# Kernel tuning notes

Measured on AMD Instinct MI355X. Metric: run time of the kernel, lower is better.

## Reference

```python
import jax, jax.numpy as jnp
import numpy as np

K = 3
TOPK = 32
TELEPORT = 0.1
LN_EPS = 1e-5


def _block(x, ln_g, ln_b, w1, b1, w2, b2, log_tau, gate):
    residual = x
    # pre: LayerNorm -> Linear -> GELU (exact erf, torch default)
    mu = jnp.mean(x, axis=-1, keepdims=True)
    var = jnp.mean(jnp.square(x - mu), axis=-1, keepdims=True)
    h = (x - mu) * jax.lax.rsqrt(var + LN_EPS) * ln_g + ln_b
    h = jax.nn.gelu(h @ w1 + b1, approximate=False)  # [B, N, H]

    # dynamic cosine adjacency with top-k sparsification
    tau = jnp.maximum(jnp.exp(log_tau), 1e-3)
    xn = h / jnp.maximum(jnp.linalg.norm(h, axis=-1, keepdims=True), 1e-12)
    A = jnp.maximum(jnp.einsum('bnf,bmf->bnm', xn, xn), 0.0)  # [B, N, N]
    B, N, _ = A.shape
    vals, idx = jax.lax.top_k(A, TOPK)  # idx: [B, N, TOPK]
    bi = jnp.arange(B)[:, None, None]
    ni = jnp.arange(N)[None, :, None]
    mask = jnp.zeros(A.shape, dtype=bool).at[bi, ni, idx].set(True)
    I = jnp.eye(N, dtype=A.dtype)
    A = jnp.where(mask, A, 0.0) + I
    A = A / tau

    # teleport + symmetric degree normalization
    A = (1.0 - TELEPORT) * A + TELEPORT * I
    deg = jnp.maximum(A.sum(-1), 1e-6)  # [B, N]
    dm12 = deg ** -0.5
    Ahat = dm12[:, :, None] * A * dm12[:, None, :]

    # Chebyshev propagation
    T0 = h
    outs = [T0]
    if K > 1:
        T1 = jnp.einsum('bnm,bmf->bnf', Ahat, T0)
        outs.append(T1)
    for _ in range(2, K):
        outs.append(2.0 * jnp.einsum('bnm,bmf->bnf', Ahat, outs[-1]) - outs[-2])
    hcat = jnp.concatenate(outs, axis=-1)  # [B, N, H*K]
    y = hcat @ w2 + b2
    return residual + jnp.tanh(gate) * y


def setup_inputs() -> dict:
    key = jax.random.key(0)
    k0, k1, k2 = jax.random.split(key, 3)
    Bsz, N, D, H, O = 4, 4096, 128, 128, 128
    x = jax.random.normal(k0, (Bsz, N, D), dtype=jnp.float32)
    ln_g = jnp.ones((D,), jnp.float32)
    ln_b = jnp.zeros((D,), jnp.float32)
    w1 = jax.random.normal(k1, (D, H), jnp.float32) / np.float32(np.sqrt(D))
    b1 = jnp.zeros((H,), jnp.float32)
    w2 = jax.random.normal(k2, (H * K, O), jnp.float32) / np.float32(np.sqrt(H * K))
    b2 = jnp.zeros((O,), jnp.float32)
    log_tau = jnp.asarray(np.log(0.5), jnp.float32)
    gate = jnp.asarray(0.2, jnp.float32)
    return {"x": x, "ln_g": ln_g, "ln_b": ln_b, "w1": w1, "b1": b1,
            "w2": w2, "b2": b2, "log_tau": log_tau, "gate": gate}


def reference(x, ln_g, ln_b, w1, b1, w2, b2, log_tau, gate):
    return _block(x, ln_g, ln_b, w1, b1, w2, b2, log_tau, gate)
```

## Files before the change

kernel.cpp:

```cpp
#include <hip/hip_runtime.h>
#include <hip/hip_bf16.h>
#include <stdint.h>

#define NB 4
#define NN 4096

using f16x8 = __attribute__((ext_vector_type(8))) _Float16;
using f32x4 = __attribute__((ext_vector_type(4))) float;

__device__ __forceinline__ float wave_sum(float v) {
  #pragma unroll
  for (int o = 32; o > 0; o >>= 1) v += __shfl_xor(v, o, 64);
  return v;
}
__device__ __forceinline__ float h2f_bits(unsigned hb) {
  unsigned short us = (unsigned short)hb;
  _Float16 hf;
  __builtin_memcpy(&hf, &us, 2);
  return (float)hf;
}
__device__ __forceinline__ unsigned short f2h_bits(float f) {
  _Float16 hf = (_Float16)f;
  unsigned short us;
  __builtin_memcpy(&us, &hf, 2);
  return us;
}
__device__ __forceinline__ unsigned pack2h(float lo, float hi) {
  return ((unsigned)f2h_bits(hi) << 16) | (unsigned)f2h_bits(lo);
}

#define INS16(c) do { unsigned t_;                      \
  t_ = max(l0, c);  c = min(l0, c);  l0 = t_;           \
  t_ = max(l1, c);  c = min(l1, c);  l1 = t_;           \
  t_ = max(l2, c);  c = min(l2, c);  l2 = t_;           \
  t_ = max(l3, c);  c = min(l3, c);  l3 = t_;           \
  t_ = max(l4, c);  c = min(l4, c);  l4 = t_;           \
  t_ = max(l5, c);  c = min(l5, c);  l5 = t_;           \
  t_ = max(l6, c);  c = min(l6, c);  l6 = t_;           \
  t_ = max(l7, c);  c = min(l7, c);  l7 = t_;           \
  t_ = max(l8, c);  c = min(l8, c);  l8 = t_;           \
  t_ = max(l9, c);  c = min(l9, c);  l9 = t_;           \
  t_ = max(l10, c); c = min(l10, c); l10 = t_;          \
  t_ = max(l11, c); c = min(l11, c); l11 = t_;          \
  t_ = max(l12, c); c = min(l12, c); l12 = t_;          \
  t_ = max(l13, c); c = min(l13, c); l13 = t_;          \
  t_ = max(l14, c); c = min(l14, c); l14 = t_;          \
  l15 = max(l15, c);                                    \
} while (0)

#define SHIFT_L() do { l0=l1; l1=l2; l2=l3; l3=l4; l4=l5; l5=l6; l6=l7; l7=l8; \
  l8=l9; l9=l10; l10=l11; l11=l12; l12=l13; l13=l14; l14=l15; l15=0; } while (0)
#define SHIFT_P() do { p0=p1; p1=p2; p2=p3; p3=p4; p4=p5; p5=p6; p6=p7; p7=p8; \
  p8=p9; p9=p10; p10=p11; p11=p12; p12=p13; p13=p14; p14=p15; p15=0; } while (0)

__global__ __launch_bounds__(128) void k_prepw(
    const float* __restrict__ w1, const float* __restrict__ w2,
    _Float16* __restrict__ w1t16, _Float16* __restrict__ w2t16) {
  int n = blockIdx.x;
  int t = threadIdx.x;
  __shared__ _Float16 v16[128];
  __shared__ float v[384];
  v16[t] = (_Float16)w1[(size_t)t * 128 + n];
  #pragma unroll
  for (int i = 0; i < 3; ++i) v[i * 128 + t] = w2[(size_t)(i * 128 + t) * 128 + n];
  __syncthreads();
  if (t < 16) {
    union { _Float16 hh[8]; uint4 u; } pk;
    #pragma unroll
    for (int j = 0; j < 8; ++j) pk.hh[j] = v16[t * 8 + j];
    *(uint4*)(w1t16 + (size_t)n * 128 + (size_t)(t ^ (n & 7)) * 8) = pk.u;
  }
  if (t < 48) {
    int kc = t >> 4, cl = t & 15;
    union { _Float16 hh[8]; uint4 u; } pk;
    #pragma unroll
    for (int e = 0; e < 8; ++e) pk.hh[e] = (_Float16)v[t * 8 + e];
    *(uint4*)(w2t16 + (size_t)n * 384 + kc * 128 + (size_t)(cl ^ (n & 7)) * 8) = pk.u;
  }
}

__global__ __launch_bounds__(256) void k0_ln(
    const float* __restrict__ x, const float* __restrict__ ln_g,
    const float* __restrict__ ln_b, _Float16* __restrict__ ln16) {
  int lane = threadIdx.x & 63;
  int row = blockIdx.x * 4 + (threadIdx.x >> 6);
  float2 xv = ((const float2*)x)[(size_t)row * 64 + lane];
  float2 gv = ((const float2*)ln_g)[lane];
  float2 bv = ((const float2*)ln_b)[lane];
  float mu = wave_sum(xv.x + xv.y) * (1.0f / 128.0f);
  float dx = xv.x - mu, dy = xv.y - mu;
  float var = wave_sum(dx * dx + dy * dy) * (1.0f / 128.0f);
  float ri = 1.0f / sqrtf(var + 1e-5f);
  float h0 = dx * ri * gv.x + bv.x;
  float h1 = dy * ri * gv.y + bv.y;
  int c = lane >> 2;
  int addr = row * 128 + ((c ^ (row & 7)) << 3) + (lane & 3) * 2;
  *(unsigned*)(ln16 + addr) = pack2h(h0, h1);
}

__global__ __launch_bounds__(256) void k1_mfma(
    const _Float16* __restrict__ ln16, const _Float16* __restrict__ w1t16,
    const float* __restrict__ b1, _Float16* __restrict__ h16,
    _Float16* __restrict__ hn16) {
  __shared__ _Float16 As[64 * 128];
  __shared__ _Float16 Bs[128 * 128];
  int tid = threadIdx.x;
  int lane = tid & 63;
  int wv = tid >> 6;
  int rbase = blockIdx.x * 64;
  #pragma unroll
  for (int i = 0; i < 4; ++i) {
    int idx = tid + 256 * i;
    __builtin_amdgcn_global_load_lds(
        (const __attribute__((address_space(1))) void*)(ln16 + (size_t)rbase * 128 + (size_t)idx * 8),
        (__attribute__((address_space(3))) void*)(As + (size_t)idx * 8), 16, 0, 0);
  }
  #pragma unroll
  for (int i = 0; i < 8; ++i) {
    int idx = tid + 256 * i;
    __builtin_amdgcn_global_load_lds(
        (const __attribute__((address_space(1))) void*)(w1t16 + (size_t)idx * 8),
        (__attribute__((address_space(3))) void*)(Bs + (size_t)idx * 8), 16, 0, 0);
  }
  asm volatile("s_waitcnt vmcnt(0)" ::: "memory");
  __syncthreads();

  int rl = lane & 15, kg = lane >> 4;
  f32x4 acc[8];
  #pragma unroll
  for (int j = 0; j < 8; ++j) acc[j] = (f32x4){0.f, 0.f, 0.f, 0.f};
  #pragma unroll
  for (int kk = 0; kk < 4; ++kk) {
    int cL = kk * 4 + kg;
    int r = wv * 16 + rl;
    f16x8 a = *(const f16x8*)(As + r * 128 + (cL ^ (r & 7)) * 8);
    #pragma unroll
    for (int j = 0; j < 8; ++j) {
      int n = j * 16 + rl;
      f16x8 bf = *(const f16x8*)(Bs + n * 128 + (cL ^ (n & 7)) * 8);
      acc[j] = __builtin_amdgcn_mfma_f32_16x16x32_f16(a, bf, acc[j], 0, 0, 0);
    }
  }
  float ssq[4] = {0.f, 0.f, 0.f, 0.f};
  #pragma unroll
  for (int j = 0; j < 8; ++j) {
    float bv = b1[j * 16 + rl];
    #pragma unroll
    for (int rg = 0; rg < 4; ++rg) {
      float z = acc[j][rg] + bv;
      float g = 0.5f * z * (1.0f + erff(z * 0.70710678118654752440f));
      acc[j][rg] = g;
      ssq[rg] += g * g;
    }
  }
  #pragma unroll
  for (int o = 1; o < 16; o <<= 1)
    #pragma unroll
    for (int rg = 0; rg < 4; ++rg) ssq[rg] += __shfl_xor(ssq[rg], o, 64);
  float rinv[4];
  #pragma unroll
  for (int rg = 0; rg < 4; ++rg) rinv[rg] = 1.0f / fmaxf(sqrtf(ssq[rg]), 1e-12f);

  #pragma unroll
  for (int j = 0; j < 8; ++j) {
    #pragma unroll
    for (int rg = 0; rg < 4; ++rg) {
      float g = acc[j][rg];
      float gp = __shfl_xor(g, 1, 64);
      if ((rl & 1) == 0) {
        int row = rbase + wv * 16 + kg * 4 + rg;
        int col = j * 16 + rl;
        int c = col >> 3;
        int ad = row * 128 + (((c ^ (row & 7))) << 3) + (col & 7);
        *(unsigned*)(h16 + ad) = pack2h(g, gp);
        *(unsigned*)(hn16 + ad) = pack2h(g * rinv[rg], gp * rinv[rg]);
      }
    }
  }
}

__global__ __launch_bounds__(512, 1) void k_scores_topk(
    const _Float16* __restrict__ hn16, int* __restrict__ nidx,
    float* __restrict__ nval, float* __restrict__ dm12,
    const float* __restrict__ p_log_tau) {
  __shared__ _Float16 Qs[64 * 128];
  __shared__ _Float16 Cs[2][2][64 * 128];
  __shared__ unsigned stk[16 * 512];
  int tid = threadIdx.x;
  int lane = tid & 63;
  int wv = tid >> 6;
  int g = wv >> 2;
  int wq = wv & 3;
  int rl = lane & 15, kg = lane >> 4;
  int t = tid & 255;
  int blk = blockIdx.x;
  int b = blk >> 6;
  int qbase = (blk & 63) * 64;
  const _Float16* hb = hn16 + (size_t)b * NN * 128;

  #pragma unroll
  for (int i = 0; i < 2; ++i) {
    int idx = tid + 512 * i;
    __builtin_amdgcn_global_load_lds(
        (const __attribute__((address_space(1))) void*)(hb + (size_t)qbase * 128 + (size_t)idx * 8),
        (__attribute__((address_space(3))) void*)(Qs + (size_t)idx * 8), 16, 0, 0);
  }
  const _Float16* cw = hb + (size_t)(g * 2048) * 128;
  #pragma unroll
  for (int i = 0; i < 4; ++i) {
    int idx = t + 256 * i;
    __builtin_amdgcn_global_load_lds(
        (const __attribute__((address_space(1))) void*)(cw + (size_t)idx * 8),
        (__attribute__((address_space(3))) void*)(&Cs[g][0][0] + (size_t)idx * 8), 16, 0, 0);
  }
  asm volatile("s_waitcnt vmcnt(0)" ::: "memory");
  __syncthreads();

  int qrow = wq * 16 + rl;
  f16x8 bq[4];
  #pragma unroll
  for (int kk = 0; kk < 4; ++kk)
    bq[kk] = *(const f16x8*)(Qs + qrow * 128 + ((kk * 4 + kg) ^ (qrow & 7)) * 8);

  unsigned l0 = 0, l1 = 0, l2 = 0, l3 = 0, l4 = 0, l5 = 0, l6 = 0, l7 = 0,
           l8 = 0, l9 = 0, l10 = 0, l11 = 0, l12 = 0, l13 = 0, l14 = 0, l15 = 0;
  unsigned gate = 0;

  for (int cb = 0; cb < 32; ++cb) {
    int cur = cb & 1;
    if (cb < 31) {
      const _Float16* csrc = cw + (size_t)(cb + 1) * 64 * 128;
      #pragma unroll
      for (int i = 0; i < 4; ++i) {
        int idx = t + 256 * i;
        __builtin_amdgcn_global_load_lds(
            (const __attribute__((address_space(1))) void*)(csrc + (size_t)idx * 8),
            (__attribute__((address_space(3))) void*)(&Cs[g][cur ^ 1][0] + (size_t)idx * 8), 16, 0, 0);
      }
    }
    f32x4 acc[4];
    #pragma unroll
    for (int j = 0; j < 4; ++j) acc[j] = (f32x4){0.f, 0.f, 0.f, 0.f};
    #pragma unroll
    for (int kk = 0; kk < 4; ++kk) {
      #pragma unroll
      for (int j = 0; j < 4; ++j) {
        int mrow = j * 16 + rl;
        f16x8 a = *(const f16x8*)(&Cs[g][cur][0] + mrow * 128 + ((kk * 4 + kg) ^ (rl & 7)) * 8);
        acc[j] = __builtin_amdgcn_mfma_f32_16x16x32_f16(a, bq[kk], acc[j], 0, 0, 0);
      }
    }
    int cnt = 0;
    int kb = 4095 - (g * 2048 + cb * 64 + kg * 4);
    #pragma unroll
    for (int j = 0; j < 4; ++j) {
      #pragma unroll
      for (int rg = 0; rg < 4; ++rg) {
        float v = fmaxf(acc[j][rg], 0.0f);
        unsigned key = ((unsigned)f2h_bits(v) << 16) | (unsigned)(kb - j * 16 - rg);
        if (key > gate) {
          stk[cnt * 512 + tid] = key;
          ++cnt;
        }
      }
    }
    int wm = cnt;
    #pragma unroll
    for (int o = 1; o < 64; o <<= 1) {
      int w = __shfl_xor(wm, o, 64);
      wm = max(wm, w);
    }
    if (wm > 0) {
      unsigned nxt = stk[tid];
      for (int i = 0; i < wm; ++i) {
        unsigned c = (i < cnt) ? nxt : 0u;
        nxt = stk[(unsigned)min(i + 1, 15) * 512 + tid];
        INS16(c);
      }
      unsigned m7 = min(l7, (unsigned)__shfl_xor((int)l7, 16, 64));
      m7 = min(m7, (unsigned)__shfl_xor((int)m7, 32, 64));
      gate = max(l15, m7);
    }
    asm volatile("s_waitcnt vmcnt(0)" ::: "memory");
    __syncthreads();
  }

  if (g == 1) {
    unsigned* dst = stk + (((wq * 16 + rl) * 4 + kg) * 16);
    *(uint4*)(dst + 0)  = (uint4){l0, l1, l2, l3};
    *(uint4*)(dst + 4)  = (uint4){l4, l5, l6, l7};
    *(uint4*)(dst + 8)  = (uint4){l8, l9, l10, l11};
    *(uint4*)(dst + 12) = (uint4){l12, l13, l14, l15};
  }
  __syncthreads();
  if (g == 0) {
    const unsigned* src = stk + (((wq * 16 + rl) * 4 + kg) * 16);
    uint4 pa = *(const uint4*)(src + 0);
    uint4 pb = *(const uint4*)(src + 4);
    uint4 pc = *(const uint4*)(src + 8);
    uint4 pd = *(const uint4*)(src + 12);
    unsigned p0 = pa.x, p1 = pa.y, p2 = pa.z, p3 = pa.w;
    unsigned p4 = pb.x, p5 = pb.y, p6 = pb.z, p7 = pb.w;
    unsigned p8 = pc.x, p9 = pc.y, p10 = pc.z, p11 = pc.w;
    unsigned p12 = pd.x, p13 = pd.y, p14 = pd.z, p15 = pd.w;

    unsigned sv[8];
    float sum = 0.0f;
    #pragma unroll
    for (int e = 0; e < 32; ++e) {
      unsigned v = max(l0, p0);
      v = max(v, (unsigned)__shfl_xor((int)v, 16, 64));
      v = max(v, (unsigned)__shfl_xor((int)v, 32, 64));
      if (l0 == v) { SHIFT_L(); }
      else if (p0 == v) { SHIFT_P(); }
      sum += h2f_bits(v >> 16);
      if (kg == (e & 3)) sv[e >> 2] = v;
    }
    int grow = b * NN + qbase + qrow;
    #pragma unroll
    for (int s = 0; s < 8; ++s) {
      unsigned v = sv[s];
      nidx[(size_t)grow * 32 + s * 4 + kg] = 4095 - (int)(v & 0xFFFu);
      nval[(size_t)grow * 32 + s * 4 + kg] = h2f_bits(v >> 16);
    }
    if (kg == 0) {
      float tau = fmaxf(expf(p_log_tau[0]), 1e-3f);
      float deg = fmaxf(0.9f * ((sum + 1.0f) / tau) + 0.1f, 1e-6f);
      dm12[grow] = 1.0f / sqrtf(deg);
    }
  }
}

__global__ __launch_bounds__(128) void k_cheb1(
    const _Float16* __restrict__ h16, const int* __restrict__ nidx,
    const float* __restrict__ nval, const float* __restrict__ dm12,
    const float* __restrict__ p_log_tau, _Float16* __restrict__ T116) {
  int row = blockIdx.x;
  int b = row >> 12;
  int tid = threadIdx.x;
  __shared__ float cj[32];
  __shared__ int mj[32];
  __shared__ float cdsh;
  float tau = fmaxf(expf(p_log_tau[0]), 1e-3f);
  float scale = 0.9f / tau;
  float dn = dm12[row];
  if (tid < 32) {
    int m = nidx[(size_t)row * 32 + tid];
    cj[tid] = scale * nval[(size_t)row * 32 + tid] * dn * dm12[b * NN + m];
    mj[tid] = m;
  }
  if (tid == 0) cdsh = (scale + 0.1f) * dn * dn;
  __syncthreads();
  int c = tid >> 3, e = tid & 7;
  const _Float16* hb = h16 + (size_t)b * NN * 128;
  float acc = cdsh * (float)h16[(size_t)row * 128 + ((c ^ (row & 7)) << 3) + e];
  #pragma unroll 8
  for (int j = 0; j < 32; ++j) {
    int m = mj[j];
    acc += cj[j] * (float)hb[(size_t)m * 128 + ((c ^ (m & 7)) << 3) + e];
  }
  float p = __shfl_xor(acc, 1, 64);
  if (!(tid & 1))
    *(unsigned*)(T116 + (size_t)row * 128 + ((c ^ (row & 7)) << 3) + e) = pack2h(acc, p);
}

__global__ __launch_bounds__(128) void k_cheb2(
    const _Float16* __restrict__ h16, const _Float16* __restrict__ T116,
    const int* __restrict__ nidx, const float* __restrict__ nval,
    const float* __restrict__ dm12, const float* __restrict__ p_log_tau,
    _Float16* __restrict__ T216) {
  int row = blockIdx.x;
  int b = row >> 12;
  int tid = threadIdx.x;
  __shared__ float cj[32];
  __shared__ int mj[32];
  __shared__ float cdsh;
  float tau = fmaxf(expf(p_log_tau[0]), 1e-3f);
  float scale = 0.9f / tau;
  float dn = dm12[row];
  if (tid < 32) {
    int m = nidx[(size_t)row * 32 + tid];
    cj[tid] = scale * nval[(size_t)row * 32 + tid] * dn * dm12[b * NN + m];
    mj[tid] = m;
  }
  if (tid == 0) cdsh = (scale + 0.1f) * dn * dn;
  __syncthreads();
  int c = tid >> 3, e = tid & 7;
  int sw_own = ((c ^ (row & 7)) << 3) + e;
  const _Float16* T1b = T116 + (size_t)b * NN * 128;
  float a = cdsh * (float)T116[(size_t)row * 128 + sw_own];
  #pragma unroll 8
  for (int j = 0; j < 32; ++j) {
    int m = mj[j];
    a += cj[j] * (float)T1b[(size_t)m * 128 + ((c ^ (m & 7)) << 3) + e];
  }
  float t2 = 2.0f * a - (float)h16[(size_t)row * 128 + sw_own];
  float p = __shfl_xor(t2, 1, 64);
  if (!(tid & 1))
    *(unsigned*)(T216 + (size_t)row * 128 + sw_own) = pack2h(t2, p);
}

__global__ __launch_bounds__(256, 1) void k_out(
    const float* __restrict__ x, const _Float16* __restrict__ h16,
    const _Float16* __restrict__ T116, const _Float16* __restrict__ T216,
    const _Float16* __restrict__ w2t16, const float* __restrict__ b2,
    const float* __restrict__ p_gate, float* __restrict__ out) {
  __shared__ _Float16 As3[3][64 * 128];
  __shared__ _Float16 Bs3[3][128 * 128];
  int tid = threadIdx.x;
  int lane = tid & 63;
  int wv = tid >> 6;
  int rbase = blockIdx.x * 64;
  const _Float16* srcs[3] = {h16, T116, T216};
  #pragma unroll
  for (int kc = 0; kc < 3; ++kc) {
    const _Float16* src = srcs[kc] + (size_t)rbase * 128;
    #pragma unroll
    for (int i = 0; i < 4; ++i) {
      int idx = tid + 256 * i;
      __builtin_amdgcn_global_load_lds(
          (const __attribute__((address_space(1))) void*)(src + (size_t)idx * 8),
          (__attribute__((address_space(3))) void*)(As3[kc] + (size_t)idx * 8), 16, 0, 0);
    }
    #pragma unroll
    for (int i = 0; i < 8; ++i) {
      int idx = tid + 256 * i;
      int n = idx >> 4, cp = idx & 15;
      __builtin_amdgcn_global_load_lds(
          (const __attribute__((address_space(1))) void*)(w2t16 + (size_t)n * 384 + kc * 128 + (size_t)cp * 8),
          (__attribute__((address_space(3))) void*)(Bs3[kc] + (size_t)idx * 8), 16, 0, 0);
    }
  }
  asm volatile("s_waitcnt vmcnt(0)" ::: "memory");
  __syncthreads();

  int rl = lane & 15, kg = lane >> 4;
  f32x4 acc[8];
  #pragma unroll
  for (int j = 0; j < 8; ++j) acc[j] = (f32x4){0.f, 0.f, 0.f, 0.f};
  #pragma unroll
  for (int kc = 0; kc < 3; ++kc) {
    #pragma unroll
    for (int kk = 0; kk < 4; ++kk) {
      int cL = kk * 4 + kg;
      int r = wv * 16 + rl;
      f16x8 a = *(const f16x8*)(As3[kc] + r * 128 + (cL ^ (r & 7)) * 8);
      #pragma unroll
      for (int j = 0; j < 8; ++j) {
        int n = j * 16 + rl;
        f16x8 bf = *(const f16x8*)(Bs3[kc] + n * 128 + (cL ^ (n & 7)) * 8);
        acc[j] = __builtin_amdgcn_mfma_f32_16x16x32_f16(a, bf, acc[j], 0, 0, 0);
      }
    }
  }
  float tg = tanhf(p_gate[0]);
  #pragma unroll
  for (int j = 0; j < 8; ++j) {
    int col = j * 16 + rl;
    float bv = b2[col];
    #pragma unroll
    for (int rg = 0; rg < 4; ++rg) {
      int row = rbase + wv * 16 + kg * 4 + rg;
      out[(size_t)row * 128 + col] =
          x[(size_t)row * 128 + col] + tg * (acc[j][rg] + bv);
    }
  }
}

extern "C" void kernel_launch(void* const* d_in, const int* in_sizes, int n_in,
                              void* d_out, int out_size, void* d_ws, size_t ws_size,
                              hipStream_t stream) {
  (void)in_sizes; (void)n_in; (void)out_size; (void)ws_size;
  const float* x = (const float*)d_in[0];
  const float* ln_g = (const float*)d_in[1];
  const float* ln_b = (const float*)d_in[2];
  const float* w1 = (const float*)d_in[3];
  const float* b1 = (const float*)d_in[4];
  const float* w2 = (const float*)d_in[5];
  const float* b2 = (const float*)d_in[6];
  const float* p_log_tau = (const float*)d_in[7];
  const float* p_gate = (const float*)d_in[8];
  float* out = (float*)d_out;

  char* ws = (char*)d_ws;
  size_t off = 0;
  auto alloc = [&](size_t bytes) -> void* {
    off = (off + 255) & ~(size_t)255;
    void* p = ws + off;
    off += bytes;
    return p;
  };
  _Float16* ln16 = (_Float16*)alloc((size_t)NB * NN * 128 * 2);
  _Float16* h16 = (_Float16*)alloc((size_t)NB * NN * 128 * 2);
  _Float16* hn16 = (_Float16*)alloc((size_t)NB * NN * 128 * 2);
  _Float16* T116 = (_Float16*)alloc((size_t)NB * NN * 128 * 2);
  _Float16* T216 = (_Float16*)alloc((size_t)NB * NN * 128 * 2);
  _Float16* w1t16 = (_Float16*)alloc((size_t)128 * 128 * 2);
  _Float16* w2t16 = (_Float16*)alloc((size_t)128 * 384 * 2);
  int* nidx = (int*)alloc((size_t)NB * NN * 32 * 4);
  float* nval = (float*)alloc((size_t)NB * NN * 32 * 4);
  float* dm12 = (float*)alloc((size_t)NB * NN * 4);

  k_prepw<<<128, 128, 0, stream>>>(w1, w2, w1t16, w2t16);
  k0_ln<<<NB * NN / 4, 256, 0, stream>>>(x, ln_g, ln_b, ln16);
  k1_mfma<<<NB * NN / 64, 256, 0, stream>>>(ln16, w1t16, b1, h16, hn16);
  k_scores_topk<<<NB * 64, 512, 0, stream>>>(hn16, nidx, nval, dm12, p_log_tau);
  k_cheb1<<<NB * NN, 128, 0, stream>>>(h16, nidx, nval, dm12, p_log_tau, T116);
  k_cheb2<<<NB * NN, 128, 0, stream>>>(h16, T116, nidx, nval, dm12, p_log_tau, T216);
  k_out<<<NB * NN / 64, 256, 0, stream>>>(x, h16, T116, T216, w2t16, b2, p_gate, out);
}
```

Baseline: 170.7 us.

## Fuse LayerNorm into first GEMM and second Chebyshev step into output GEMM

LayerNorm is now computed inside the first MFMA kernel, which writes fp16 rows straight into LDS, so the ln16 buffer and its kernel launch go away. The second Chebyshev propagation moves into the output GEMM kernel: neighbour weights are staged in LDS, T2 is built in LDS from gathered T1 rows, and the T216 buffer and k_cheb2 launch are removed. The top-k insertion loop replaces a wave-wide max reduction with ballot-based early exit. In exchange, k_out does the gather work with one block per 64 rows and uses more LDS, which can reduce parallelism for that irregular gather.

```diff
diff --git a/kernel.cpp b/kernel.cpp
--- a/kernel.cpp
+++ b/kernel.cpp
@@ -79,27 +79,9 @@
   }
 }
 
-__global__ __launch_bounds__(256) void k0_ln(
+__global__ __launch_bounds__(256) void k1_mfma(
     const float* __restrict__ x, const float* __restrict__ ln_g,
-    const float* __restrict__ ln_b, _Float16* __restrict__ ln16) {
-  int lane = threadIdx.x & 63;
-  int row = blockIdx.x * 4 + (threadIdx.x >> 6);
-  float2 xv = ((const float2*)x)[(size_t)row * 64 + lane];
-  float2 gv = ((const float2*)ln_g)[lane];
-  float2 bv = ((const float2*)ln_b)[lane];
-  float mu = wave_sum(xv.x + xv.y) * (1.0f / 128.0f);
-  float dx = xv.x - mu, dy = xv.y - mu;
-  float var = wave_sum(dx * dx + dy * dy) * (1.0f / 128.0f);
-  float ri = 1.0f / sqrtf(var + 1e-5f);
-  float h0 = dx * ri * gv.x + bv.x;
-  float h1 = dy * ri * gv.y + bv.y;
-  int c = lane >> 2;
-  int addr = row * 128 + ((c ^ (row & 7)) << 3) + (lane & 3) * 2;
-  *(unsigned*)(ln16 + addr) = pack2h(h0, h1);
-}
-
-__global__ __launch_bounds__(256) void k1_mfma(
-    const _Float16* __restrict__ ln16, const _Float16* __restrict__ w1t16,
+    const float* __restrict__ ln_b, const _Float16* __restrict__ w1t16,
     const float* __restrict__ b1, _Float16* __restrict__ h16,
     _Float16* __restrict__ hn16) {
   __shared__ _Float16 As[64 * 128];
@@ -109,19 +91,52 @@
   int wv = tid >> 6;
   int rbase = blockIdx.x * 64;
   #pragma unroll
-  for (int i = 0; i < 4; ++i) {
-    int idx = tid + 256 * i;
-    __builtin_amdgcn_global_load_lds(
-        (const __attribute__((address_space(1))) void*)(ln16 + (size_t)rbase * 128 + (size_t)idx * 8),
-        (__attribute__((address_space(3))) void*)(As + (size_t)idx * 8), 16, 0, 0);
-  }
-  #pragma unroll
   for (int i = 0; i < 8; ++i) {
     int idx = tid + 256 * i;
     __builtin_amdgcn_global_load_lds(
         (const __attribute__((address_space(1))) void*)(w1t16 + (size_t)idx * 8),
         (__attribute__((address_space(3))) void*)(Bs + (size_t)idx * 8), 16, 0, 0);
   }
+  int r = wv * 16 + (lane >> 2);
+  int q = lane & 3;
+  const float4* xr = (const float4*)(x + (size_t)(rbase + r) * 128 + q * 32);
+  float4 xv[8];
+  #pragma unroll
+  for (int j = 0; j < 8; ++j) xv[j] = xr[j];
+  float s = 0.f;
+  #pragma unroll
+  for (int j = 0; j < 8; ++j) s += xv[j].x + xv[j].y + xv[j].z + xv[j].w;
+  s += __shfl_xor(s, 1, 64);
+  s += __shfl_xor(s, 2, 64);
+  float mu = s * (1.0f / 128.0f);
+  float vs = 0.f;
+  #pragma unroll
+  for (int j = 0; j < 8; ++j) {
+    float dx_ = xv[j].x - mu, dy_ = xv[j].y - mu, dz_ = xv[j].z - mu, dw_ = xv[j].w - mu;
+    vs += dx_ * dx_ + dy_ * dy_ + dz_ * dz_ + dw_ * dw_;
+  }
+  vs += __shfl_xor(vs, 1, 64);
+  vs += __shfl_xor(vs, 2, 64);
+  float ri = 1.0f / sqrtf(vs * (1.0f / 128.0f) + 1e-5f);
+  const float4* gr = (const float4*)(ln_g + q * 32);
+  const float4* br = (const float4*)(ln_b + q * 32);
+  #pragma unroll
+  for (int cc = 0; cc < 4; ++cc) {
+    float4 a0 = xv[cc * 2], a1 = xv[cc * 2 + 1];
+    float4 g0 = gr[cc * 2], g1 = gr[cc * 2 + 1];
+    float4 bb0 = br[cc * 2], bb1 = br[cc * 2 + 1];
+    union { _Float16 hh[8]; uint4 u; } pk;
+    pk.hh[0] = (_Float16)((a0.x - mu) * ri * g0.x + bb0.x);
+    pk.hh[1] = (_Float16)((a0.y - mu) * ri * g0.y + bb0.y);
+    pk.hh[2] = (_Float16)((a0.z - mu) * ri * g0.z + bb0.z);
+    pk.hh[3] = (_Float16)((a0.w - mu) * ri * g0.w + bb0.w);
+    pk.hh[4] = (_Float16)((a1.x - mu) * ri * g1.x + bb1.x);
+    pk.hh[5] = (_Float16)((a1.y - mu) * ri * g1.y + bb1.y);
+    pk.hh[6] = (_Float16)((a1.z - mu) * ri * g1.z + bb1.z);
+    pk.hh[7] = (_Float16)((a1.w - mu) * ri * g1.w + bb1.w);
+    int c = q * 4 + cc;
+    *(uint4*)(&As[r * 128 + ((c ^ (r & 7)) << 3)]) = pk.u;
+  }
   asm volatile("s_waitcnt vmcnt(0)" ::: "memory");
   __syncthreads();
 
@@ -132,8 +147,8 @@
   #pragma unroll
   for (int kk = 0; kk < 4; ++kk) {
     int cL = kk * 4 + kg;
-    int r = wv * 16 + rl;
-    f16x8 a = *(const f16x8*)(As + r * 128 + (cL ^ (r & 7)) * 8);
+    int rr = wv * 16 + rl;
+    f16x8 a = *(const f16x8*)(As + rr * 128 + (cL ^ (rr & 7)) * 8);
     #pragma unroll
     for (int j = 0; j < 8; ++j) {
       int n = j * 16 + rl;
@@ -264,15 +279,10 @@
         }
       }
     }
-    int wm = cnt;
-    #pragma unroll
-    for (int o = 1; o < 64; o <<= 1) {
-      int w = __shfl_xor(wm, o, 64);
-      wm = max(wm, w);
-    }
-    if (wm > 0) {
+    if (__ballot(cnt > 0) != 0ull) {
       unsigned nxt = stk[tid];
-      for (int i = 0; i < wm; ++i) {
+      for (int i = 0;; ++i) {
+        if (__ballot(i < cnt) == 0ull) break;
         unsigned c = (i < cnt) ? nxt : 0u;
         nxt = stk[(unsigned)min(i + 1, 15) * 512 + tid];
         INS16(c);
@@ -364,56 +374,26 @@
     *(unsigned*)(T116 + (size_t)row * 128 + ((c ^ (row & 7)) << 3) + e) = pack2h(acc, p);
 }
 
-__global__ __launch_bounds__(128) void k_cheb2(
-    const _Float16* __restrict__ h16, const _Float16* __restrict__ T116,
-    const int* __restrict__ nidx, const float* __restrict__ nval,
-    const float* __restrict__ dm12, const float* __restrict__ p_log_tau,
-    _Float16* __restrict__ T216) {
-  int row = blockIdx.x;
-  int b = row >> 12;
-  int tid = threadIdx.x;
-  __shared__ float cj[32];
-  __shared__ int mj[32];
-  __shared__ float cdsh;
-  float tau = fmaxf(expf(p_log_tau[0]), 1e-3f);
-  float scale = 0.9f / tau;
-  float dn = dm12[row];
-  if (tid < 32) {
-    int m = nidx[(size_t)row * 32 + tid];
-    cj[tid] = scale * nval[(size_t)row * 32 + tid] * dn * dm12[b * NN + m];
-    mj[tid] = m;
-  }
-  if (tid == 0) cdsh = (scale + 0.1f) * dn * dn;
-  __syncthreads();
-  int c = tid >> 3, e = tid & 7;
-  int sw_own = ((c ^ (row & 7)) << 3) + e;
-  const _Float16* T1b = T116 + (size_t)b * NN * 128;
-  float a = cdsh * (float)T116[(size_t)row * 128 + sw_own];
-  #pragma unroll 8
-  for (int j = 0; j < 32; ++j) {
-    int m = mj[j];
-    a += cj[j] * (float)T1b[(size_t)m * 128 + ((c ^ (m & 7)) << 3) + e];
-  }
-  float t2 = 2.0f * a - (float)h16[(size_t)row * 128 + sw_own];
-  float p = __shfl_xor(t2, 1, 64);
-  if (!(tid & 1))
-    *(unsigned*)(T216 + (size_t)row * 128 + sw_own) = pack2h(t2, p);
-}
-
 __global__ __launch_bounds__(256, 1) void k_out(
     const float* __restrict__ x, const _Float16* __restrict__ h16,
-    const _Float16* __restrict__ T116, const _Float16* __restrict__ T216,
-    const _Float16* __restrict__ w2t16, const float* __restrict__ b2,
-    const float* __restrict__ p_gate, float* __restrict__ out) {
+    const _Float16* __restrict__ T116, const _Float16* __restrict__ w2t16,
+    const float* __restrict__ b2, const int* __restrict__ nidx,
+    const float* __restrict__ nval, const float* __restrict__ dm12,
+    const float* __restrict__ p_log_tau, const float* __restrict__ p_gate,
+    float* __restrict__ out) {
   __shared__ _Float16 As3[3][64 * 128];
   __shared__ _Float16 Bs3[3][128 * 128];
+  __shared__ float cjs[64][32];
+  __shared__ unsigned short mjs[64][32];
+  __shared__ float cds[64];
   int tid = threadIdx.x;
   int lane = tid & 63;
   int wv = tid >> 6;
   int rbase = blockIdx.x * 64;
-  const _Float16* srcs[3] = {h16, T116, T216};
-  #pragma unroll
-  for (int kc = 0; kc < 3; ++kc) {
+  int b = rbase >> 12;
+  const _Float16* srcs[2] = {h16, T116};
+  #pragma unroll
+  for (int kc = 0; kc < 2; ++kc) {
     const _Float16* src = srcs[kc] + (size_t)rbase * 128;
     #pragma unroll
     for (int i = 0; i < 4; ++i) {
@@ -422,6 +402,9 @@
           (const __attribute__((address_space(1))) void*)(src + (size_t)idx * 8),
           (__attribute__((address_space(3))) void*)(As3[kc] + (size_t)idx * 8), 16, 0, 0);
     }
+  }
+  #pragma unroll
+  for (int kc = 0; kc < 3; ++kc) {
     #pragma unroll
     for (int i = 0; i < 8; ++i) {
       int idx = tid + 256 * i;
@@ -431,7 +414,43 @@
           (__attribute__((address_space(3))) void*)(Bs3[kc] + (size_t)idx * 8), 16, 0, 0);
     }
   }
+  float tau = fmaxf(expf(p_log_tau[0]), 1e-3f);
+  float scale = 0.9f / tau;
+  #pragma unroll
+  for (int i = 0; i < 8; ++i) {
+    int idx = tid + 256 * i;
+    int row = idx >> 5, j = idx & 31;
+    int grow = rbase + row;
+    int m = nidx[(size_t)grow * 32 + j];
+    float dn = dm12[grow];
+    cjs[row][j] = scale * nval[(size_t)grow * 32 + j] * dn * dm12[b * NN + m];
+    mjs[row][j] = (unsigned short)m;
+    if (j == 0) cds[row] = (scale + 0.1f) * dn * dn;
+  }
   asm volatile("s_waitcnt vmcnt(0)" ::: "memory");
+  __syncthreads();
+
+  const _Float16* T1g = T116 + (size_t)b * NN * 128;
+  #pragma unroll 2
+  for (int p = 0; p < 16; ++p) {
+    int r = p * 4 + (tid >> 6);
+    int e0 = (tid & 63) * 2;
+    int c0 = e0 >> 3;
+    int own = r * 128 + ((c0 ^ (r & 7)) << 3) + (e0 & 7);
+    float acc0 = cds[r] * (float)As3[1][own];
+    float acc1 = cds[r] * (float)As3[1][own + 1];
+    #pragma unroll 8
+    for (int j = 0; j < 32; ++j) {
+      int m = mjs[r][j];
+      float cj = cjs[r][j];
+      unsigned u = *(const unsigned*)(T1g + (size_t)m * 128 + ((c0 ^ (m & 7)) << 3) + (e0 & 7));
+      acc0 += cj * h2f_bits(u & 0xFFFFu);
+      acc1 += cj * h2f_bits(u >> 16);
+    }
+    float t2a = 2.0f * acc0 - (float)As3[0][own];
+    float t2b = 2.0f * acc1 - (float)As3[0][own + 1];
+    *(unsigned*)(&As3[2][own]) = pack2h(t2a, t2b);
+  }
   __syncthreads();
 
   int rl = lane & 15, kg = lane >> 4;
@@ -490,11 +509,9 @@
     off += bytes;
     return p;
   };
-  _Float16* ln16 = (_Float16*)alloc((size_t)NB * NN * 128 * 2);
   _Float16* h16 = (_Float16*)alloc((size_t)NB * NN * 128 * 2);
   _Float16* hn16 = (_Float16*)alloc((size_t)NB * NN * 128 * 2);
   _Float16* T116 = (_Float16*)alloc((size_t)NB * NN * 128 * 2);
-  _Float16* T216 = (_Float16*)alloc((size_t)NB * NN * 128 * 2);
   _Float16* w1t16 = (_Float16*)alloc((size_t)128 * 128 * 2);
   _Float16* w2t16 = (_Float16*)alloc((size_t)128 * 384 * 2);
   int* nidx = (int*)alloc((size_t)NB * NN * 32 * 4);
@@ -502,10 +519,9 @@
   float* dm12 = (float*)alloc((size_t)NB * NN * 4);
 
   k_prepw<<<128, 128, 0, stream>>>(w1, w2, w1t16, w2t16);
-  k0_ln<<<NB * NN / 4, 256, 0, stream>>>(x, ln_g, ln_b, ln16);
-  k1_mfma<<<NB * NN / 64, 256, 0, stream>>>(ln16, w1t16, b1, h16, hn16);
+  k1_mfma<<<NB * NN / 64, 256, 0, stream>>>(x, ln_g, ln_b, w1t16, b1, h16, hn16);
   k_scores_topk<<<NB * 64, 512, 0, stream>>>(hn16, nidx, nval, dm12, p_log_tau);
   k_cheb1<<<NB * NN, 128, 0, stream>>>(h16, nidx, nval, dm12, p_log_tau, T116);
-  k_cheb2<<<NB * NN, 128, 0, stream>>>(h16, T116, nidx, nval, dm12, p_log_tau, T216);
-  k_out<<<NB * NN / 64, 256, 0, stream>>>(x, h16, T116, T216, w2t16, b2, p_gate, out);
-}
+  k_out<<<NB * NN / 64, 256, 0, stream>>>(x, h16, T116, w2t16, b2, nidx, nval,
+                                          dm12, p_log_tau, p_gate, out);
+}
```

After: 184.2 us. 1.08x slower.

## Split top-k scoring across candidate halves and merge partial top-k in new kernel

Applied to the files above, without the earlier changes.

The score/top-k kernel now splits the 4096 candidate columns into two halves per query tile, doubling the grid from 256 to 512 blocks and shrinking the candidate tile to 32 rows. Each half writes its partial top-32 keys to a new buffer, and a new merge kernel picks the final top-32 per row and computes the degree normalization. The intent is to fill more CUs on a 256-CU part and allow higher occupancy via smaller LDS. The cost is an extra launch plus a round trip of the partial keys through global memory.

```diff
diff --git a/kernel.cpp b/kernel.cpp
--- a/kernel.cpp
+++ b/kernel.cpp
@@ -179,12 +179,10 @@
   }
 }
 
-__global__ __launch_bounds__(512, 1) void k_scores_topk(
-    const _Float16* __restrict__ hn16, int* __restrict__ nidx,
-    float* __restrict__ nval, float* __restrict__ dm12,
-    const float* __restrict__ p_log_tau) {
+__global__ __launch_bounds__(512, 4) void k_scores_topk(
+    const _Float16* __restrict__ hn16, unsigned* __restrict__ pnk) {
   __shared__ _Float16 Qs[64 * 128];
-  __shared__ _Float16 Cs[2][2][64 * 128];
+  __shared__ _Float16 Cs[2][2][32 * 128];
   __shared__ unsigned stk[16 * 512];
   int tid = threadIdx.x;
   int lane = tid & 63;
@@ -194,8 +192,10 @@
   int rl = lane & 15, kg = lane >> 4;
   int t = tid & 255;
   int blk = blockIdx.x;
-  int b = blk >> 6;
-  int qbase = (blk & 63) * 64;
+  int b = blk >> 7;
+  int rem = blk & 127;
+  int qbase = (rem >> 1) * 64;
+  int mh = rem & 1;
   const _Float16* hb = hn16 + (size_t)b * NN * 128;
 
   #pragma unroll
@@ -205,9 +205,9 @@
         (const __attribute__((address_space(1))) void*)(hb + (size_t)qbase * 128 + (size_t)idx * 8),
         (__attribute__((address_space(3))) void*)(Qs + (size_t)idx * 8), 16, 0, 0);
   }
-  const _Float16* cw = hb + (size_t)(g * 2048) * 128;
-  #pragma unroll
-  for (int i = 0; i < 4; ++i) {
+  const _Float16* cw = hb + (size_t)(mh * 2048 + g * 1024) * 128;
+  #pragma unroll
+  for (int i = 0; i < 2; ++i) {
     int idx = t + 256 * i;
     __builtin_amdgcn_global_load_lds(
         (const __attribute__((address_space(1))) void*)(cw + (size_t)idx * 8),
@@ -229,31 +229,31 @@
   for (int cb = 0; cb < 32; ++cb) {
     int cur = cb & 1;
     if (cb < 31) {
-      const _Float16* csrc = cw + (size_t)(cb + 1) * 64 * 128;
+      const _Float16* csrc = cw + (size_t)(cb + 1) * 32 * 128;
       #pragma unroll
-      for (int i = 0; i < 4; ++i) {
+      for (int i = 0; i < 2; ++i) {
         int idx = t + 256 * i;
         __builtin_amdgcn_global_load_lds(
             (const __attribute__((address_space(1))) void*)(csrc + (size_t)idx * 8),
             (__attribute__((address_space(3))) void*)(&Cs[g][cur ^ 1][0] + (size_t)idx * 8), 16, 0, 0);
       }
     }
-    f32x4 acc[4];
-    #pragma unroll
-    for (int j = 0; j < 4; ++j) acc[j] = (f32x4){0.f, 0.f, 0.f, 0.f};
+    f32x4 acc[2];
+    #pragma unroll
+    for (int j = 0; j < 2; ++j) acc[j] = (f32x4){0.f, 0.f, 0.f, 0.f};
     #pragma unroll
     for (int kk = 0; kk < 4; ++kk) {
       #pragma unroll
-      for (int j = 0; j < 4; ++j) {
+      for (int j = 0; j < 2; ++j) {
         int mrow = j * 16 + rl;
         f16x8 a = *(const f16x8*)(&Cs[g][cur][0] + mrow * 128 + ((kk * 4 + kg) ^ (rl & 7)) * 8);
         acc[j] = __builtin_amdgcn_mfma_f32_16x16x32_f16(a, bq[kk], acc[j], 0, 0, 0);
       }
     }
     int cnt = 0;
-    int kb = 4095 - (g * 2048 + cb * 64 + kg * 4);
-    #pragma unroll
-    for (int j = 0; j < 4; ++j) {
+    int kb = 4095 - (mh * 2048 + g * 1024 + cb * 32 + kg * 4);
+    #pragma unroll
+    for (int j = 0; j < 2; ++j) {
       #pragma unroll
       for (int rg = 0; rg < 4; ++rg) {
         float v = fmaxf(acc[j][rg], 0.0f);
@@ -305,7 +305,6 @@
     unsigned p12 = pd.x, p13 = pd.y, p14 = pd.z, p15 = pd.w;
 
     unsigned sv[8];
-    float sum = 0.0f;
     #pragma unroll
     for (int e = 0; e < 32; ++e) {
       unsigned v = max(l0, p0);
@@ -313,21 +312,44 @@
       v = max(v, (unsigned)__shfl_xor((int)v, 32, 64));
       if (l0 == v) { SHIFT_L(); }
       else if (p0 == v) { SHIFT_P(); }
-      sum += h2f_bits(v >> 16);
       if (kg == (e & 3)) sv[e >> 2] = v;
     }
     int grow = b * NN + qbase + qrow;
-    #pragma unroll
-    for (int s = 0; s < 8; ++s) {
-      unsigned v = sv[s];
-      nidx[(size_t)grow * 32 + s * 4 + kg] = 4095 - (int)(v & 0xFFFu);
-      nval[(size_t)grow * 32 + s * 4 + kg] = h2f_bits(v >> 16);
-    }
-    if (kg == 0) {
-      float tau = fmaxf(expf(p_log_tau[0]), 1e-3f);
-      float deg = fmaxf(0.9f * ((sum + 1.0f) / tau) + 0.1f, 1e-6f);
-      dm12[grow] = 1.0f / sqrtf(deg);
-    }
+    unsigned* dst = pnk + (size_t)grow * 64 + mh * 32;
+    #pragma unroll
+    for (int s = 0; s < 8; ++s) dst[s * 4 + kg] = sv[s];
+  }
+}
+
+__global__ __launch_bounds__(256) void k_topk_merge(
+    const unsigned* __restrict__ pnk, int* __restrict__ nidx,
+    float* __restrict__ nval, float* __restrict__ dm12,
+    const float* __restrict__ p_log_tau) {
+  int lane = threadIdx.x & 63;
+  int q = blockIdx.x * 4 + (threadIdx.x >> 6);
+  unsigned k0 = pnk[(size_t)q * 64 + lane];
+  float sum = 0.0f;
+  unsigned myv = 0;
+  #pragma unroll
+  for (int e = 0; e < 32; ++e) {
+    unsigned v = k0;
+    #pragma unroll
+    for (int o = 32; o > 0; o >>= 1) {
+      unsigned w = (unsigned)__shfl_xor((int)v, o, 64);
+      v = max(v, w);
+    }
+    if (k0 == v) k0 = 0;
+    sum += h2f_bits(v >> 16);
+    if (lane == e) myv = v;
+  }
+  if (lane < 32) {
+    nidx[(size_t)q * 32 + lane] = 4095 - (int)(myv & 0xFFFu);
+    nval[(size_t)q * 32 + lane] = h2f_bits(myv >> 16);
+  }
+  if (lane == 0) {
+    float tau = fmaxf(expf(p_log_tau[0]), 1e-3f);
+    float deg = fmaxf(0.9f * ((sum + 1.0f) / tau) + 0.1f, 1e-6f);
+    dm12[q] = 1.0f / sqrtf(deg);
   }
 }
 
@@ -500,11 +522,13 @@
   int* nidx = (int*)alloc((size_t)NB * NN * 32 * 4);
   float* nval = (float*)alloc((size_t)NB * NN * 32 * 4);
   float* dm12 = (float*)alloc((size_t)NB * NN * 4);
+  unsigned* pnk = (unsigned*)alloc((size_t)NB * NN * 64 * 4);
 
   k_prepw<<<128, 128, 0, stream>>>(w1, w2, w1t16, w2t16);
   k0_ln<<<NB * NN / 4, 256, 0, stream>>>(x, ln_g, ln_b, ln16);
   k1_mfma<<<NB * NN / 64, 256, 0, stream>>>(ln16, w1t16, b1, h16, hn16);
-  k_scores_topk<<<NB * 64, 512, 0, stream>>>(hn16, nidx, nval, dm12, p_log_tau);
+  k_scores_topk<<<NB * 128, 512, 0, stream>>>(hn16, pnk);
+  k_topk_merge<<<NB * NN / 4, 256, 0, stream>>>(pnk, nidx, nval, dm12, p_log_tau);
   k_cheb1<<<NB * NN, 128, 0, stream>>>(h16, nidx, nval, dm12, p_log_tau, T116);
   k_cheb2<<<NB * NN, 128, 0, stream>>>(h16, T116, nidx, nval, dm12, p_log_tau, T216);
   k_out<<<NB * NN / 64, 256, 0, stream>>>(x, h16, T116, T216, w2t16, b2, p_gate, out);
```

After: 205.9 us. +20.7%, slower.
